# Kernel tuning notes

Measured on AMD Instinct MI355X. Metric: run time of the kernel, lower is better.

## Reference

```python
import jax, jax.numpy as jnp
import numpy as np

STATE = 300
CAUSE = 40
PATCH = 16
N_PATCH = 4
GAMMA0 = 0.2


def _norm_cols(w):
    # torch: w / w.norm(dim=2, keepdim=True) on (1,1,r,c) -> normalize over rows
    return w / jnp.linalg.norm(w, axis=0, keepdims=True)[None, :][0]


def setup_inputs() -> dict:
    key = jax.random.key(0)
    kX, kU, kx0, kA, kB, kC = jax.random.split(key, 6)
    B, T = 256, 64
    X = jax.random.normal(kX, (B, N_PATCH, STATE, 1, T), dtype=jnp.float32)
    U = jax.random.normal(kU, (B, 1, CAUSE, 1, T), dtype=jnp.float32)
    x0 = jax.random.normal(kx0, (B, N_PATCH, STATE, 1), dtype=jnp.float32)
    # parameters: uniform then column-normalized over dim=2 (row axis), as in __init__
    A = jax.random.uniform(kA, (STATE, STATE), dtype=jnp.float32)
    A = A / jnp.linalg.norm(A, axis=0, keepdims=True)
    Bm = jax.random.uniform(kB, (STATE, CAUSE), dtype=jnp.float32)
    Bm = Bm / jnp.linalg.norm(Bm, axis=0, keepdims=True)
    C = jax.random.uniform(kC, (PATCH * PATCH, STATE), dtype=jnp.float32)
    C = C / jnp.linalg.norm(C, axis=0, keepdims=True)
    return {"X": X, "U": U, "x0": x0, "A": A, "Bm": Bm, "C": C}


def reference(X, U, x0, A, Bm, C):
    # X: (B, 4, 300, 1, T); U: (B, 1, 40, 1, T); x0: (B, 4, 300, 1)
    Bsz, npatch, _, _, T = X.shape
    # x_prev sequence: [x0, X[...,0], ..., X[...,T-2]]
    X_prev = jnp.concatenate([x0[..., None], X[..., :-1]], axis=-1)
    # X_pred[t] = A @ x_prev_t   -> (B, 4, 300, 1, T)
    X_pred = jnp.einsum('ij,bpjkt->bpikt', A, X_prev)
    # recon[t] = C @ x_t -> (B, 4, 256, 1, T)
    recon = jnp.einsum('ij,bpjkt->bpikt', C, X)
    # patch_to_image, vectorized over trailing T: grid 2x2 of 16x16 patches -> 32x32
    gs = int(np.sqrt(npatch))
    img = recon.reshape(Bsz, gs, gs, 1, PATCH, PATCH, T)
    img = img.transpose(0, 3, 1, 4, 2, 5, 6)
    vid_recon = img.reshape(Bsz, 1, gs * PATCH, gs * PATCH, T)
    # cause state: gamma0*(1+exp(-B@u))/2 * sum_p |x|
    Bu = jnp.einsum('ij,bojkt->boikt', Bm, U)           # (B,1,300,1,T)
    gamma = GAMMA0 * (1.0 + jnp.exp(-Bu)) * 0.5
    X_U = gamma * jnp.sum(jnp.abs(X), axis=1, keepdims=True)  # (B,1,300,1,T)
    return vid_recon, X_pred, X_U
```

## Files before the change

### kernel.cpp

```cpp
#include <hip/hip_runtime.h>

#define STATE  300
#define TDIM   64
#define NCAUSE 40
#define NP     4
#define KPAD   320
#define ROWB   (KPAD*2)
#define LDS_HALF (65*ROWB)
#define NT_A   19
#define NT_C   16
#define WS_NEEDED 716800u

typedef float f32x4 __attribute__((ext_vector_type(4)));
typedef short s16x8 __attribute__((ext_vector_type(8)));

static __device__ __forceinline__ ushort f2bf(float f) {
    uint x = __float_as_uint(f);
    x += 0x7fffu + ((x >> 16) & 1u);
    return (ushort)(x >> 16);
}
static __device__ __forceinline__ float bf2f(ushort u) {
    return __uint_as_float(((uint)u) << 16);
}

__global__ void prep_kernel(const float* __restrict__ A, const float* __restrict__ C,
                            ushort* __restrict__ ws) {
    const int it   = blockIdx.x;
    const int ks   = blockIdx.y;
    const int lane = threadIdx.x;
    const bool isA = (it < NT_A);
    const float* __restrict__ W = isA ? A : C;
    const int M   = isA ? STATE : 256;
    const int itl = isA ? it : it - NT_A;
    const int row = itl*16 + (lane & 15);
    const int k0  = ks*32 + (lane >> 4)*8;

    ushort hv[8], lv[8];
    #pragma unroll
    for (int j = 0; j < 8; ++j) {
        const int k = k0 + j;
        float v = 0.f;
        if (row < M && k < STATE) v = W[row*STATE + k];
        const ushort h = f2bf(v);
        hv[j] = h;
        lv[j] = f2bf(v - bf2f(h));
    }
    const int plane = (isA ? NT_A : NT_C)*10*64*8;
    ushort* hb = ws + (isA ? 0 : 2*NT_A*10*64*8) + ((itl*10 + ks)*64 + lane)*8;
    ushort* lb = hb + plane;
    #pragma unroll
    for (int j = 0; j < 8; ++j) { hb[j] = hv[j]; lb[j] = lv[j]; }
}

#define DO_TT(ACC, TT_, PHOFF) { \
    const int tp  = (TT_)*16 + c + (PHOFF); \
    const int off = (tp*ROWB + kbyte) ^ ((tp & 7) << 4); \
    const s16x8 bh = *(const s16x8*)(Xs + off); \
    const s16x8 bl = *(const s16x8*)(Xs + off + LDS_HALF); \
    ACC = __builtin_amdgcn_mfma_f32_16x16x32_bf16(ah, bh, ACC, 0, 0, 0); \
    ACC = __builtin_amdgcn_mfma_f32_16x16x32_bf16(ah, bl, ACC, 0, 0, 0); \
    ACC = __builtin_amdgcn_mfma_f32_16x16x32_bf16(al, bh, ACC, 0, 0, 0); \
}

__global__ __launch_bounds__(512, 1)
void pred_recon_mfma(const float* __restrict__ X, const float* __restrict__ x0,
                     const ushort* __restrict__ ws,
                     float* __restrict__ vid, float* __restrict__ Xpred) {
    __shared__ __align__(16) char Xs[2*LDS_HALF];
    const int bp   = blockIdx.x;
    const int tid  = threadIdx.x;
    const int lane = tid & 63;
    const int w    = tid >> 6;

    const float* __restrict__ Xbp = X + (size_t)bp*(STATE*TDIM);
    #pragma unroll 1
    for (int i = 0; i < 10; ++i) {
        const int k4 = w + 8*i;
        if (k4 < 75) {
            const int k = k4*4;
            const int t = lane;
            const float v0 = Xbp[(k+0)*TDIM + t];
            const float v1 = Xbp[(k+1)*TDIM + t];
            const float v2 = Xbp[(k+2)*TDIM + t];
            const float v3 = Xbp[(k+3)*TDIM + t];
            const ushort h0 = f2bf(v0), h1 = f2bf(v1), h2 = f2bf(v2), h3 = f2bf(v3);
            uint2 hp, lp;
            hp.x = (uint)h0 | ((uint)h1 << 16);
            hp.y = (uint)h2 | ((uint)h3 << 16);
            lp.x = (uint)f2bf(v0 - bf2f(h0)) | ((uint)f2bf(v1 - bf2f(h1)) << 16);
            lp.y = (uint)f2bf(v2 - bf2f(h2)) | ((uint)f2bf(v3 - bf2f(h3)) << 16);
            const int tp  = t + 1;
            const int off = (tp*ROWB + k*2) ^ ((tp & 7) << 4);
            *(uint2*)(Xs + off)            = hp;
            *(uint2*)(Xs + off + LDS_HALF) = lp;
        }
    }
    const float* __restrict__ x0bp = x0 + (size_t)bp*STATE;
    for (int k = tid; k < STATE; k += 512) {
        const float v = x0bp[k];
        const ushort h = f2bf(v);
        *(ushort*)(Xs + k*2)            = h;
        *(ushort*)(Xs + k*2 + LDS_HALF) = f2bf(v - bf2f(h));
    }
    for (int idx = tid; idx < 130; idx += 512) {
        const int h = idx / 65, tp = idx % 65;
        char* base = Xs + h*LDS_HALF;
        const int sw = (tp & 7) << 4;
        uint2 z; z.x = 0u; z.y = 0u;
        #pragma unroll
        for (int j = 0; j < 5; ++j)
            *(uint2*)(base + ((tp*ROWB + 600 + j*8) ^ sw)) = z;
    }
    __syncthreads();

    const int c  = lane & 15;
    const int kg = lane >> 4;
    const ushort* __restrict__ Af_h = ws;
    const ushort* __restrict__ Af_l = Af_h + NT_A*10*64*8;
    const ushort* __restrict__ Cf_h = Af_l + NT_A*10*64*8;
    const ushort* __restrict__ Cf_l = Cf_h + NT_C*10*64*8;

    {
        float* __restrict__ outp = Xpred + (size_t)bp*(STATE*TDIM);
        #pragma unroll 1
        for (int it = w; it < NT_A; it += 8) {
            f32x4 a0 = {0,0,0,0}, a1 = {0,0,0,0}, a2 = {0,0,0,0}, a3 = {0,0,0,0};
            #pragma unroll 2
            for (int ks = 0; ks < 10; ++ks) {
                const int kbyte = ks*64 + kg*16;
                const s16x8 ah = *(const s16x8*)(Af_h + ((it*10 + ks)*64 + lane)*8);
                const s16x8 al = *(const s16x8*)(Af_l + ((it*10 + ks)*64 + lane)*8);
                DO_TT(a0, 0, 0) DO_TT(a1, 1, 0) DO_TT(a2, 2, 0) DO_TT(a3, 3, 0)
            }
            #pragma unroll
            for (int r = 0; r < 4; ++r) {
                const int row = it*16 + kg*4 + r;
                if (row < STATE) {
                    outp[row*TDIM +  0 + c] = a0[r];
                    outp[row*TDIM + 16 + c] = a1[r];
                    outp[row*TDIM + 32 + c] = a2[r];
                    outp[row*TDIM + 48 + c] = a3[r];
                }
            }
        }
    }

    {
        const int b = bp >> 2, p = bp & 3, gr = p >> 1, gc = p & 1;
        float* __restrict__ vb = vid + (size_t)b*(32*32*TDIM)
                                     + (size_t)(gr*16)*(32*TDIM)
                                     + (size_t)(gc*16)*TDIM;
        #pragma unroll 1
        for (int it = w; it < NT_C; it += 8) {
            f32x4 a0 = {0,0,0,0}, a1 = {0,0,0,0}, a2 = {0,0,0,0}, a3 = {0,0,0,0};
            #pragma unroll 2
            for (int ks = 0; ks < 10; ++ks) {
                const int kbyte = ks*64 + kg*16;
                const s16x8 ah = *(const s16x8*)(Cf_h + ((it*10 + ks)*64 + lane)*8);
                const s16x8 al = *(const s16x8*)(Cf_l + ((it*10 + ks)*64 + lane)*8);
                DO_TT(a0, 0, 1) DO_TT(a1, 1, 1) DO_TT(a2, 2, 1) DO_TT(a3, 3, 1)
            }
            #pragma unroll
            for (int r = 0; r < 4; ++r) {
                const int pc = kg*4 + r;
                float* vr = vb + it*(32*TDIM) + pc*TDIM;
                vr[ 0 + c] = a0[r];
                vr[16 + c] = a1[r];
                vr[32 + c] = a2[r];
                vr[48 + c] = a3[r];
            }
        }
    }
}

__global__ __launch_bounds__(256)
void xu_kernel(const float* __restrict__ X, const float* __restrict__ U,
               const float* __restrict__ Bm, float* __restrict__ XU) {
    __shared__ float gl[60*68];
    const int b    = blockIdx.y;
    const int sg   = blockIdx.x;
    const int tid  = threadIdx.x;
    const int lane = tid & 63;
    const int w    = __builtin_amdgcn_readfirstlane(tid >> 6);

    const float* __restrict__ Ub = U + (size_t)b*(NCAUSE*TDIM);
    float u[40];
    #pragma unroll
    for (int k = 0; k < 40; ++k) u[k] = Ub[k*TDIM + lane];

    const int sbase = sg*60;
    const int s0    = w*15;
    #pragma unroll 1
    for (int r = 0; r < 15; ++r) {
        const float* __restrict__ brow = Bm + (size_t)(sbase + s0 + r)*NCAUSE;
        float bu = 0.f;
        #pragma unroll
        for (int q = 0; q < 10; ++q) {
            const float4 m = *(const float4*)(brow + q*4);
            bu += m.x*u[4*q] + m.y*u[4*q+1] + m.z*u[4*q+2] + m.w*u[4*q+3];
        }
        gl[(s0 + r)*68 + lane] = 0.1f*(1.f + __expf(-bu));
    }
    __syncthreads();

    const float* __restrict__ Xb  = X  + (size_t)b*(NP*STATE*TDIM);
    float* __restrict__ XUb       = XU + (size_t)b*(STATE*TDIM);
    #pragma unroll 1
    for (int idx = tid; idx < 60*16; idx += 256) {
        const int sp = idx >> 4, t4 = idx & 15;
        const int s  = sbase + sp;
        const float4 g = *(const float4*)(gl + sp*68 + t4*4);
        float4 a; a.x = 0.f; a.y = 0.f; a.z = 0.f; a.w = 0.f;
        #pragma unroll
        for (int p = 0; p < NP; ++p) {
            const float4 xv = *(const float4*)(Xb + ((size_t)p*STATE + s)*TDIM + t4*4);
            a.x += fabsf(xv.x); a.y += fabsf(xv.y); a.z += fabsf(xv.z); a.w += fabsf(xv.w);
        }
        float4 o; o.x = g.x*a.x; o.y = g.y*a.y; o.z = g.z*a.z; o.w = g.w*a.w;
        *(float4*)(XUb + (size_t)s*TDIM + t4*4) = o;
    }
}

__global__ __launch_bounds__(256, 2)
void pred_recon_f32(const float* __restrict__ X, const float* __restrict__ x0,
                    const float* __restrict__ A, const float* __restrict__ C,
                    float* __restrict__ vid, float* __restrict__ Xpred) {
    __shared__ float Xsf[STATE*65];
    const int bp = blockIdx.x, tid = threadIdx.x;
    const float* Xbp = X + (size_t)bp*(STATE*TDIM);
    const float* x0bp = x0 + (size_t)bp*STATE;
    for (int idx = tid; idx < STATE*65; idx += 256) {
        const int k = idx/65, tp = idx - k*65;
        Xsf[idx] = (tp == 0) ? x0bp[k] : Xbp[k*TDIM + (tp-1)];
    }
    __syncthreads();
    const int t = tid & 63, rg = tid >> 6;
    float* outp = Xpred + (size_t)bp*(STATE*TDIM);
    for (int chunk = 0; chunk < 15; ++chunk) {
        const int i0 = rg*75 + chunk*5;
        float acc[5] = {0,0,0,0,0};
        for (int k4 = 0; k4 < STATE/4; ++k4) {
            const int kb = k4*4;
            const float x0v = Xsf[(kb+0)*65 + t], x1v = Xsf[(kb+1)*65 + t];
            const float x2v = Xsf[(kb+2)*65 + t], x3v = Xsf[(kb+3)*65 + t];
            #pragma unroll
            for (int r = 0; r < 5; ++r) {
                const float4 a = *(const float4*)(A + (size_t)(i0+r)*STATE + kb);
                acc[r] += a.x*x0v + a.y*x1v + a.z*x2v + a.w*x3v;
            }
        }
        #pragma unroll
        for (int r = 0; r < 5; ++r) outp[(i0+r)*TDIM + t] = acc[r];
    }
    const int b = bp >> 2, p = bp & 3, gr = p >> 1, gc = p & 1;
    float* vb = vid + (size_t)b*(32*32*TDIM) + (size_t)(gr*16)*(32*TDIM) + (size_t)(gc*16)*TDIM;
    for (int chunk = 0; chunk < 16; ++chunk) {
        const int i0 = rg*64 + chunk*4;
        float acc[4] = {0,0,0,0};
        for (int k4 = 0; k4 < STATE/4; ++k4) {
            const int kb = k4*4;
            const float x0v = Xsf[(kb+0)*65 + (t+1)], x1v = Xsf[(kb+1)*65 + (t+1)];
            const float x2v = Xsf[(kb+2)*65 + (t+1)], x3v = Xsf[(kb+3)*65 + (t+1)];
            #pragma unroll
            for (int r = 0; r < 4; ++r) {
                const float4 cc = *(const float4*)(C + (size_t)(i0+r)*STATE + kb);
                acc[r] += cc.x*x0v + cc.y*x1v + cc.z*x2v + cc.w*x3v;
            }
        }
        #pragma unroll
        for (int r = 0; r < 4; ++r) {
            const int i = i0 + r;
            vb[(i >> 4)*(32*TDIM) + (i & 15)*TDIM + t] = acc[r];
        }
    }
}

extern "C" void kernel_launch(void* const* d_in, const int* in_sizes, int n_in,
                              void* d_out, int out_size, void* d_ws, size_t ws_size,
                              hipStream_t stream) {
    const float* X  = (const float*)d_in[0];
    const float* U  = (const float*)d_in[1];
    const float* x0 = (const float*)d_in[2];
    const float* A  = (const float*)d_in[3];
    const float* Bm = (const float*)d_in[4];
    const float* C  = (const float*)d_in[5];

    float* out   = (float*)d_out;
    float* vid   = out;
    float* Xpred = out + 16777216;
    float* XU    = out + 16777216 + 19660800;

    if (ws_size >= WS_NEEDED) {
        ushort* wsu = (ushort*)d_ws;
        hipLaunchKernelGGL(prep_kernel, dim3(NT_A + NT_C, 10), dim3(64), 0, stream,
                           A, C, wsu);
        hipLaunchKernelGGL(pred_recon_mfma, dim3(256*NP), dim3(512), 0, stream,
                           X, x0, wsu, vid, Xpred);
    } else {
        hipLaunchKernelGGL(pred_recon_f32, dim3(256*NP), dim3(256), 0, stream,
                           X, x0, A, C, vid, Xpred);
    }
    hipLaunchKernelGGL(xu_kernel, dim3(5, 256), dim3(256), 0, stream,
                       X, U, Bm, XU);
}
```

Measured before the change: 342.2 us.

## Split time axis across blocks and use 2x2 register-tiled MFMA with balanced waves

The pred/recon kernel now launches two 256-thread blocks per batch-patch, each handling half of the 64 time steps. The second half takes its shifted previous state from X at t=31 instead of x0. Each wave computes 2x2 output tiles, so every A/C fragment and LDS B fragment is reused twice. Row tiles are assigned in contiguous, roughly equal ranges across the four waves, and launch bounds change to allow three blocks per CU with a smaller LDS footprint. The goals are more parallelism, better occupancy and less redundant fragment loading. The cost is extra per-block setup and reloading the weight fragments for each time half.

```diff
diff --git a/kernel.cpp b/kernel.cpp
--- a/kernel.cpp
+++ b/kernel.cpp
@@ -6,7 +6,8 @@
 #define NP     4
 #define KPAD   320
 #define ROWB   (KPAD*2)
-#define LDS_HALF (65*ROWB)
+#define NROWS  33
+#define LDS_HALF (NROWS*ROWB)
 #define NT_A   19
 #define NT_C   16
 #define WS_NEEDED 716800u
@@ -52,122 +53,184 @@
     for (int j = 0; j < 8; ++j) { hb[j] = hv[j]; lb[j] = lv[j]; }
 }
 
-#define DO_TT(ACC, TT_, PHOFF) { \
-    const int tp  = (TT_)*16 + c + (PHOFF); \
-    const int off = (tp*ROWB + kbyte) ^ ((tp & 7) << 4); \
-    const s16x8 bh = *(const s16x8*)(Xs + off); \
-    const s16x8 bl = *(const s16x8*)(Xs + off + LDS_HALF); \
-    ACC = __builtin_amdgcn_mfma_f32_16x16x32_bf16(ah, bh, ACC, 0, 0, 0); \
-    ACC = __builtin_amdgcn_mfma_f32_16x16x32_bf16(ah, bl, ACC, 0, 0, 0); \
-    ACC = __builtin_amdgcn_mfma_f32_16x16x32_bf16(al, bh, ACC, 0, 0, 0); \
-}
-
-__global__ __launch_bounds__(512, 1)
+#define MFMA_(A_,B_,C_) __builtin_amdgcn_mfma_f32_16x16x32_bf16((A_),(B_),(C_),0,0,0)
+
+static __device__ __forceinline__ s16x8 ldA(const ushort* __restrict__ base, int it, int ks, int lane) {
+    return *(const s16x8*)(base + ((it*10 + ks)*64 + lane)*8);
+}
+static __device__ __forceinline__ void ldB(const char* Xs, int lr, int kbyte, s16x8& bh, s16x8& bl) {
+    const int off = (lr*ROWB + kbyte) ^ ((lr & 7) << 4);
+    bh = *(const s16x8*)(Xs + off);
+    bl = *(const s16x8*)(Xs + off + LDS_HALF);
+}
+
+template<int PHOFF>
+static __device__ __forceinline__ void gemm2(const char* Xs,
+        const ushort* __restrict__ Wh, const ushort* __restrict__ Wl,
+        int it0, int it1, int lane, int kg, int c,
+        f32x4& a00, f32x4& a01, f32x4& a10, f32x4& a11) {
+    #pragma unroll 2
+    for (int ks = 0; ks < 10; ++ks) {
+        const s16x8 ah0 = ldA(Wh, it0, ks, lane);
+        const s16x8 al0 = ldA(Wl, it0, ks, lane);
+        const s16x8 ah1 = ldA(Wh, it1, ks, lane);
+        const s16x8 al1 = ldA(Wl, it1, ks, lane);
+        const int kbyte = ks*64 + kg*16;
+        s16x8 bh0, bl0, bh1, bl1;
+        ldB(Xs, c + PHOFF,      kbyte, bh0, bl0);
+        ldB(Xs, 16 + c + PHOFF, kbyte, bh1, bl1);
+        a00 = MFMA_(ah0, bh0, a00); a00 = MFMA_(ah0, bl0, a00); a00 = MFMA_(al0, bh0, a00);
+        a01 = MFMA_(ah0, bh1, a01); a01 = MFMA_(ah0, bl1, a01); a01 = MFMA_(al0, bh1, a01);
+        a10 = MFMA_(ah1, bh0, a10); a10 = MFMA_(ah1, bl0, a10); a10 = MFMA_(al1, bh0, a10);
+        a11 = MFMA_(ah1, bh1, a11); a11 = MFMA_(ah1, bl1, a11); a11 = MFMA_(al1, bh1, a11);
+    }
+}
+
+template<int PHOFF>
+static __device__ __forceinline__ void gemm1(const char* Xs,
+        const ushort* __restrict__ Wh, const ushort* __restrict__ Wl,
+        int it0, int lane, int kg, int c, f32x4& a00, f32x4& a01) {
+    #pragma unroll 2
+    for (int ks = 0; ks < 10; ++ks) {
+        const s16x8 ah0 = ldA(Wh, it0, ks, lane);
+        const s16x8 al0 = ldA(Wl, it0, ks, lane);
+        const int kbyte = ks*64 + kg*16;
+        s16x8 bh0, bl0, bh1, bl1;
+        ldB(Xs, c + PHOFF,      kbyte, bh0, bl0);
+        ldB(Xs, 16 + c + PHOFF, kbyte, bh1, bl1);
+        a00 = MFMA_(ah0, bh0, a00); a00 = MFMA_(ah0, bl0, a00); a00 = MFMA_(al0, bh0, a00);
+        a01 = MFMA_(ah0, bh1, a01); a01 = MFMA_(ah0, bl1, a01); a01 = MFMA_(al0, bh1, a01);
+    }
+}
+
+__global__ __launch_bounds__(256, 3)
 void pred_recon_mfma(const float* __restrict__ X, const float* __restrict__ x0,
                      const ushort* __restrict__ ws,
                      float* __restrict__ vid, float* __restrict__ Xpred) {
     __shared__ __align__(16) char Xs[2*LDS_HALF];
     const int bp   = blockIdx.x;
+    const int th   = blockIdx.y;
     const int tid  = threadIdx.x;
     const int lane = tid & 63;
     const int w    = tid >> 6;
 
     const float* __restrict__ Xbp = X + (size_t)bp*(STATE*TDIM);
-    #pragma unroll 1
-    for (int i = 0; i < 10; ++i) {
-        const int k4 = w + 8*i;
-        if (k4 < 75) {
-            const int k = k4*4;
-            const int t = lane;
-            const float v0 = Xbp[(k+0)*TDIM + t];
-            const float v1 = Xbp[(k+1)*TDIM + t];
-            const float v2 = Xbp[(k+2)*TDIM + t];
-            const float v3 = Xbp[(k+3)*TDIM + t];
-            const ushort h0 = f2bf(v0), h1 = f2bf(v1), h2 = f2bf(v2), h3 = f2bf(v3);
-            uint2 hp, lp;
-            hp.x = (uint)h0 | ((uint)h1 << 16);
-            hp.y = (uint)h2 | ((uint)h3 << 16);
-            lp.x = (uint)f2bf(v0 - bf2f(h0)) | ((uint)f2bf(v1 - bf2f(h1)) << 16);
-            lp.y = (uint)f2bf(v2 - bf2f(h2)) | ((uint)f2bf(v3 - bf2f(h3)) << 16);
-            const int tp  = t + 1;
-            const int off = (tp*ROWB + k*2) ^ ((tp & 7) << 4);
-            *(uint2*)(Xs + off)            = hp;
-            *(uint2*)(Xs + off + LDS_HALF) = lp;
-        }
-    }
-    const float* __restrict__ x0bp = x0 + (size_t)bp*STATE;
-    for (int k = tid; k < STATE; k += 512) {
-        const float v = x0bp[k];
-        const ushort h = f2bf(v);
-        *(ushort*)(Xs + k*2)            = h;
-        *(ushort*)(Xs + k*2 + LDS_HALF) = f2bf(v - bf2f(h));
-    }
-    for (int idx = tid; idx < 130; idx += 512) {
-        const int h = idx / 65, tp = idx % 65;
-        char* base = Xs + h*LDS_HALF;
-        const int sw = (tp & 7) << 4;
+    {
+        const int t_lo = tid & 31;
+        const int kh   = tid >> 5;
+        const int tg   = th*32 + t_lo;
+        const int lr   = t_lo + 1;
+        const int sw   = (lr & 7) << 4;
+        #pragma unroll 1
+        for (int i = 0; i < 10; ++i) {
+            const int k4 = kh + 8*i;
+            if (k4 < 75) {
+                const int k = k4*4;
+                const float v0 = Xbp[(k+0)*TDIM + tg];
+                const float v1 = Xbp[(k+1)*TDIM + tg];
+                const float v2 = Xbp[(k+2)*TDIM + tg];
+                const float v3 = Xbp[(k+3)*TDIM + tg];
+                const ushort h0 = f2bf(v0), h1 = f2bf(v1), h2 = f2bf(v2), h3 = f2bf(v3);
+                uint2 hp, lp;
+                hp.x = (uint)h0 | ((uint)h1 << 16);
+                hp.y = (uint)h2 | ((uint)h3 << 16);
+                lp.x = (uint)f2bf(v0 - bf2f(h0)) | ((uint)f2bf(v1 - bf2f(h1)) << 16);
+                lp.y = (uint)f2bf(v2 - bf2f(h2)) | ((uint)f2bf(v3 - bf2f(h3)) << 16);
+                const int off = (lr*ROWB + k*2) ^ sw;
+                *(uint2*)(Xs + off)            = hp;
+                *(uint2*)(Xs + off + LDS_HALF) = lp;
+            }
+        }
+    }
+    if (th == 0) {
+        const float* __restrict__ x0bp = x0 + (size_t)bp*STATE;
+        for (int k = tid; k < STATE; k += 256) {
+            const float v = x0bp[k];
+            const ushort h = f2bf(v);
+            *(ushort*)(Xs + k*2)            = h;
+            *(ushort*)(Xs + k*2 + LDS_HALF) = f2bf(v - bf2f(h));
+        }
+    } else {
+        for (int k = tid; k < STATE; k += 256) {
+            const float v = Xbp[k*TDIM + 31];
+            const ushort h = f2bf(v);
+            *(ushort*)(Xs + k*2)            = h;
+            *(ushort*)(Xs + k*2 + LDS_HALF) = f2bf(v - bf2f(h));
+        }
+    }
+    for (int idx = tid; idx < 2*NROWS; idx += 256) {
+        const int plane = idx & 1, lr = idx >> 1;
+        char* base = Xs + plane*LDS_HALF;
+        const int sw = (lr & 7) << 4;
         uint2 z; z.x = 0u; z.y = 0u;
         #pragma unroll
         for (int j = 0; j < 5; ++j)
-            *(uint2*)(base + ((tp*ROWB + 600 + j*8) ^ sw)) = z;
+            *(uint2*)(base + ((lr*ROWB + 600 + j*8) ^ sw)) = z;
     }
     __syncthreads();
 
     const int c  = lane & 15;
     const int kg = lane >> 4;
+    const int tbase = th*32;
     const ushort* __restrict__ Af_h = ws;
     const ushort* __restrict__ Af_l = Af_h + NT_A*10*64*8;
     const ushort* __restrict__ Cf_h = Af_l + NT_A*10*64*8;
     const ushort* __restrict__ Cf_l = Cf_h + NT_C*10*64*8;
 
+    const int ps = (w*9 < NT_A) ? w*9 : NT_A;
+    const int pe = (ps + 9 < NT_A) ? ps + 9 : NT_A;
+    const int rs = (w < 3) ? 0 : 8;
+    const int re = (w < 2) ? 0 : (w - 1)*8;
+
     {
         float* __restrict__ outp = Xpred + (size_t)bp*(STATE*TDIM);
-        #pragma unroll 1
-        for (int it = w; it < NT_A; it += 8) {
-            f32x4 a0 = {0,0,0,0}, a1 = {0,0,0,0}, a2 = {0,0,0,0}, a3 = {0,0,0,0};
-            #pragma unroll 2
-            for (int ks = 0; ks < 10; ++ks) {
-                const int kbyte = ks*64 + kg*16;
-                const s16x8 ah = *(const s16x8*)(Af_h + ((it*10 + ks)*64 + lane)*8);
-                const s16x8 al = *(const s16x8*)(Af_l + ((it*10 + ks)*64 + lane)*8);
-                DO_TT(a0, 0, 0) DO_TT(a1, 1, 0) DO_TT(a2, 2, 0) DO_TT(a3, 3, 0)
-            }
+        int it = ps;
+        for (; it + 1 < pe; it += 2) {
+            f32x4 a00 = {0,0,0,0}, a01 = {0,0,0,0}, a10 = {0,0,0,0}, a11 = {0,0,0,0};
+            gemm2<0>(Xs, Af_h, Af_l, it, it+1, lane, kg, c, a00, a01, a10, a11);
+            #pragma unroll
+            for (int r = 0; r < 4; ++r) {
+                const int row0 = it*16 + kg*4 + r;
+                const int row1 = row0 + 16;
+                outp[row0*TDIM + tbase + c]      = a00[r];
+                outp[row0*TDIM + tbase + 16 + c] = a01[r];
+                if (row1 < STATE) {
+                    outp[row1*TDIM + tbase + c]      = a10[r];
+                    outp[row1*TDIM + tbase + 16 + c] = a11[r];
+                }
+            }
+        }
+        if (it < pe) {
+            f32x4 a00 = {0,0,0,0}, a01 = {0,0,0,0};
+            gemm1<0>(Xs, Af_h, Af_l, it, lane, kg, c, a00, a01);
             #pragma unroll
             for (int r = 0; r < 4; ++r) {
                 const int row = it*16 + kg*4 + r;
                 if (row < STATE) {
-                    outp[row*TDIM +  0 + c] = a0[r];
-                    outp[row*TDIM + 16 + c] = a1[r];
-                    outp[row*TDIM + 32 + c] = a2[r];
-                    outp[row*TDIM + 48 + c] = a3[r];
+                    outp[row*TDIM + tbase + c]      = a00[r];
+                    outp[row*TDIM + tbase + 16 + c] = a01[r];
                 }
             }
         }
     }
 
-    {
+    if (rs < re) {
         const int b = bp >> 2, p = bp & 3, gr = p >> 1, gc = p & 1;
         float* __restrict__ vb = vid + (size_t)b*(32*32*TDIM)
                                      + (size_t)(gr*16)*(32*TDIM)
                                      + (size_t)(gc*16)*TDIM;
-        #pragma unroll 1
-        for (int it = w; it < NT_C; it += 8) {
-            f32x4 a0 = {0,0,0,0}, a1 = {0,0,0,0}, a2 = {0,0,0,0}, a3 = {0,0,0,0};
-            #pragma unroll 2
-            for (int ks = 0; ks < 10; ++ks) {
-                const int kbyte = ks*64 + kg*16;
-                const s16x8 ah = *(const s16x8*)(Cf_h + ((it*10 + ks)*64 + lane)*8);
-                const s16x8 al = *(const s16x8*)(Cf_l + ((it*10 + ks)*64 + lane)*8);
-                DO_TT(a0, 0, 1) DO_TT(a1, 1, 1) DO_TT(a2, 2, 1) DO_TT(a3, 3, 1)
-            }
+        for (int it = rs; it + 1 < re + 1; it += 2) {
+            f32x4 a00 = {0,0,0,0}, a01 = {0,0,0,0}, a10 = {0,0,0,0}, a11 = {0,0,0,0};
+            gemm2<1>(Xs, Cf_h, Cf_l, it, it+1, lane, kg, c, a00, a01, a10, a11);
             #pragma unroll
             for (int r = 0; r < 4; ++r) {
                 const int pc = kg*4 + r;
-                float* vr = vb + it*(32*TDIM) + pc*TDIM;
-                vr[ 0 + c] = a0[r];
-                vr[16 + c] = a1[r];
-                vr[32 + c] = a2[r];
-                vr[48 + c] = a3[r];
+                float* vr0 = vb + (it  )*(32*TDIM) + pc*TDIM + tbase;
+                float* vr1 = vb + (it+1)*(32*TDIM) + pc*TDIM + tbase;
+                vr0[c]      = a00[r];
+                vr0[16 + c] = a01[r];
+                vr1[c]      = a10[r];
+                vr1[16 + c] = a11[r];
             }
         }
     }
@@ -294,7 +357,7 @@
         ushort* wsu = (ushort*)d_ws;
         hipLaunchKernelGGL(prep_kernel, dim3(NT_A + NT_C, 10), dim3(64), 0, stream,
                            A, C, wsu);
-        hipLaunchKernelGGL(pred_recon_mfma, dim3(256*NP), dim3(512), 0, stream,
+        hipLaunchKernelGGL(pred_recon_mfma, dim3(256*NP, 2), dim3(256), 0, stream,
                            X, x0, wsu, vid, Xpred);
     } else {
         hipLaunchKernelGGL(pred_recon_f32, dim3(256*NP), dim3(256), 0, stream,
```

Result: faster. 317.3 us (-7.3%).
